# Kernel optimization log

Hardware: AMD Instinct MI355X
Metric: run time of the kernel (lower is better)

Reference implementation:

```python
import jax, jax.numpy as jnp
import numpy as np

HID = 2048
NKH, NVH = 16, 32
DK, DV = 128, 128
KCONV = 4
KEY_DIM = NKH * DK          # 2048
VAL_DIM = NVH * DV          # 4096
CONV_DIM = 2 * KEY_DIM + VAL_DIM  # 8192
QKVZ_DIM = 2 * KEY_DIM + 2 * VAL_DIM  # 12288
R = NVH // NKH              # 2
BA_DIM = 2 * NVH            # 64
EPS = 1e-6


def _l2norm(x, eps=1e-6):
    return x * jax.lax.rsqrt(jnp.sum(x * x, axis=-1, keepdims=True) + eps)


def setup_inputs() -> dict:
    key = jax.random.key(0)
    ks = jax.random.split(key, 8)
    std = 0.02
    return {
        "hidden_states": jax.random.normal(ks[0], (2, 2048, HID), dtype=jnp.float32),
        "attention_mask": jnp.ones((2, 2048), dtype=jnp.float32),
        "W_qkvz": jax.random.normal(ks[1], (HID, QKVZ_DIM), dtype=jnp.float32) * std,
        "W_ba": jax.random.normal(ks[2], (HID, BA_DIM), dtype=jnp.float32) * std,
        "conv_kernel": jax.random.normal(ks[3], (KCONV, 1, CONV_DIM), dtype=jnp.float32) * 0.1,
        "A_log": jnp.log(jax.random.uniform(ks[4], (NVH,), dtype=jnp.float32, minval=1.0, maxval=16.0)),
        "dt_bias": jnp.ones((NVH,), dtype=jnp.float32),
        "norm_kernel": jnp.ones((DV,), dtype=jnp.float32),
        "W_out": jax.random.normal(ks[5], (VAL_DIM, HID), dtype=jnp.float32) * std,
    }


def reference(hidden_states, attention_mask, W_qkvz, W_ba, conv_kernel, A_log, dt_bias, norm_kernel, W_out):
    b, s, _ = hidden_states.shape
    h = hidden_states * attention_mask[:, :, None]  # apply padding mask

    # projections
    qkvz = h @ W_qkvz  # (b, s, QKVZ_DIM)
    ba = h @ W_ba      # (b, s, BA_DIM)

    # fix_query_key_value_ordering: grouped per-k-head layout [q, k, v*R, z*R]
    qkvz = qkvz.reshape(b, s, NKH, 2 * DK + 2 * R * DV)
    q = qkvz[..., :DK]                                   # (b,s,NKH,DK)
    k = qkvz[..., DK:2 * DK]                             # (b,s,NKH,DK)
    v = qkvz[..., 2 * DK:2 * DK + R * DV].reshape(b, s, NVH, DV)
    z = qkvz[..., 2 * DK + R * DV:].reshape(b, s, NVH, DV)
    ba = ba.reshape(b, s, NKH, 2 * R)
    beta = ba[..., :R].reshape(b, s, NVH)
    alpha = ba[..., R:].reshape(b, s, NVH)

    # causal depthwise conv over [q|k|v] channels
    conv_in = jnp.concatenate(
        [q.reshape(b, s, -1), k.reshape(b, s, -1), v.reshape(b, s, -1)], axis=-1)  # (b,s,CONV_DIM)
    conv_out = jax.lax.conv_general_dilated(
        conv_in, conv_kernel, window_strides=(1,), padding=((KCONV - 1, 0),),
        dimension_numbers=("NWC", "WIO", "NWC"), feature_group_count=CONV_DIM)
    conv_out = jax.nn.silu(conv_out)

    q = conv_out[..., :KEY_DIM].reshape(b, s, NKH, DK)
    k = conv_out[..., KEY_DIM:2 * KEY_DIM].reshape(b, s, NKH, DK)
    v = conv_out[..., 2 * KEY_DIM:].reshape(b, s, NVH, DV)

    # expand k-heads to v-heads (repeat_interleave)
    q = jnp.repeat(q, R, axis=2)  # (b,s,NVH,DK)
    k = jnp.repeat(k, R, axis=2)

    # gated delta rule parameters
    g = -jnp.exp(A_log)[None, None, :] * jax.nn.softplus(alpha + dt_bias[None, None, :])  # (b,s,NVH)
    beta = jax.nn.sigmoid(beta)
    q = _l2norm(q) * (DK ** -0.5)
    k = _l2norm(k)

    # recurrence: S_t = exp(g_t) * S_{t-1} + k_t (v_t - k_t^T S) beta_t ; o_t = q_t^T S_t
    def step(S, x):
        q_t, k_t, v_t, g_t, b_t = x
        S = S * jnp.exp(g_t)[..., None, None]               # (b,h,DK,DV)
        kv = jnp.einsum("bhk,bhkv->bhv", k_t, S)
        delta = (v_t - kv) * b_t[..., None]
        S = S + jnp.einsum("bhk,bhv->bhkv", k_t, delta)
        o_t = jnp.einsum("bhk,bhkv->bhv", q_t, S)
        return S, o_t

    xs = (q.transpose(1, 0, 2, 3), k.transpose(1, 0, 2, 3), v.transpose(1, 0, 2, 3),
          g.transpose(1, 0, 2), beta.transpose(1, 0, 2))
    S0 = jnp.zeros((b, NVH, DK, DV), dtype=hidden_states.dtype)
    _, o = jax.lax.scan(step, S0, xs)
    o = o.transpose(1, 0, 2, 3)  # (b,s,NVH,DV)

    # gated RMSNorm per head (fp32 math as in Qwen3NextRMSNormGated)
    of = o.astype(jnp.float32)
    var = jnp.mean(of * of, axis=-1, keepdims=True)
    of = of * jax.lax.rsqrt(var + EPS)
    of = norm_kernel * of
    of = of * jax.nn.silu(z.astype(jnp.float32))
    o = of.astype(o.dtype).reshape(b, s, VAL_DIM)

    return o @ W_out
```

## Files before the change

kernel.cpp:

```cpp
#include <hip/hip_runtime.h>
#include <stdint.h>

typedef float    f32x4 __attribute__((ext_vector_type(4)));
typedef float    f32x2 __attribute__((ext_vector_type(2)));
typedef _Float16 f16x8 __attribute__((ext_vector_type(8)));
typedef _Float16 f16x4 __attribute__((ext_vector_type(4)));
typedef _Float16 f16x2 __attribute__((ext_vector_type(2)));

#define SEQ   2048
#define HIDD  2048
#define MROWS 4096
#define NQKV  12288
#define NCHUNK 32
#define CLEN   64

__device__ __forceinline__ void gload_lds16(const void* g, void* l) {
  __builtin_amdgcn_global_load_lds((const __attribute__((address_space(1))) uint32_t*)g,
                                   (__attribute__((address_space(3))) uint32_t*)l, 16, 0, 0);
}
__device__ __forceinline__ int swz256(int row, int colb) { return row * 256 + (colb ^ ((row & 7) << 4)); }
__device__ __forceinline__ int swz128(int row, int colb) { return row * 128 + (colb ^ ((row & 7) << 4)); }

__global__ __launch_bounds__(256)
void amask_kernel(const float* __restrict__ h, const float* __restrict__ mask,
                  _Float16* __restrict__ A1) {
  int i = blockIdx.x * 256 + threadIdx.x;
  if (i >= MROWS * HIDD / 4) return;
  f32x4 x = ((const f32x4*)h)[i];
  float m = mask[(i * 4) >> 11];
  f16x4 r;
  r[0] = (_Float16)(x[0] * m); r[1] = (_Float16)(x[1] * m);
  r[2] = (_Float16)(x[2] * m); r[3] = (_Float16)(x[3] * m);
  *(f16x4*)(A1 + (size_t)i * 4) = r;
}

__global__ __launch_bounds__(256)
void transpose_f16(const float* __restrict__ in, _Float16* __restrict__ out,
                   int R, int C) {
  __shared__ float tile[64][65];
  int c0 = blockIdx.x * 64, r0 = blockIdx.y * 64;
  int tx = threadIdx.x & 63, ty = threadIdx.x >> 6;
  #pragma unroll
  for (int i = 0; i < 16; ++i) {
    int r = i * 4 + ty;
    tile[r][tx] = in[(size_t)(r0 + r) * C + c0 + tx];
  }
  __syncthreads();
  #pragma unroll
  for (int i = 0; i < 16; ++i) {
    int c = i * 4 + ty;
    out[(size_t)(c0 + c) * R + r0 + tx] = (_Float16)tile[tx][c];
  }
}

template <typename CT>
__global__ __launch_bounds__(256, 2)
void gemm_f16(const _Float16* __restrict__ A, const _Float16* __restrict__ Bt,
              CT* __restrict__ C, int M, int N, int K, int tiles_n) {
  __shared__ _Float16 lsA[128 * 32];
  __shared__ _Float16 lsB[128 * 32];
  int bm = blockIdx.x / tiles_n, bn = blockIdx.x % tiles_n;
  int m0 = bm * 128, n0 = bn * 128;
  int lane = threadIdx.x & 63, wid = threadIdx.x >> 6;
  int wr = wid >> 1, wc = wid & 1;
  int la = lane & 15, lk = lane >> 4;
  int ldrow = lane >> 2;
  int ldcol = (lane & 3) * 8;
  f32x4 acc[4][4] = {};
  for (int k0 = 0; k0 < K; k0 += 32) {
    __syncthreads();
    #pragma unroll
    for (int si = 0; si < 2; ++si) {
      int seg = wid * 2 + si;
      int row = seg * 16 + ldrow;
      gload_lds16(A  + (size_t)(m0 + row) * K + k0 + ldcol, &lsA[seg * 512]);
      gload_lds16(Bt + (size_t)(n0 + row) * K + k0 + ldcol, &lsB[seg * 512]);
    }
    __syncthreads();
    f16x8 af[4], bf[4];
    #pragma unroll
    for (int f = 0; f < 4; ++f) {
      af[f] = *(const f16x8*)&lsA[(wr * 64 + f * 16 + la) * 32 + lk * 8];
      bf[f] = *(const f16x8*)&lsB[(wc * 64 + f * 16 + la) * 32 + lk * 8];
    }
    #pragma unroll
    for (int i = 0; i < 4; ++i)
      #pragma unroll
      for (int j = 0; j < 4; ++j)
        acc[i][j] = __builtin_amdgcn_mfma_f32_16x16x32_f16(af[i], bf[j], acc[i][j], 0, 0, 0);
  }
  #pragma unroll
  for (int i = 0; i < 4; ++i)
    #pragma unroll
    for (int j = 0; j < 4; ++j) {
      int col = n0 + wc * 64 + j * 16 + la;
      #pragma unroll
      for (int r = 0; r < 4; ++r) {
        int row = m0 + wr * 64 + i * 16 + lk * 4 + r;
        C[(size_t)row * N + col] = (CT)acc[i][j][r];
      }
    }
}

__global__ __launch_bounds__(256)
void ba_gemm(const float* __restrict__ h, const float* __restrict__ mask,
             const float* __restrict__ Wba, float* __restrict__ ba) {
  __shared__ float red[4][8][64];
  int r0 = blockIdx.x * 8;
  int c = threadIdx.x & 63, kc = threadIdx.x >> 6;
  float acc[8] = {};
  const float* wp = Wba + (size_t)(kc * 512) * 64 + c;
  const float* hp = h + (size_t)r0 * HIDD + kc * 512;
  for (int i = 0; i < 512; ++i) {
    float w = wp[(size_t)i * 64];
    #pragma unroll
    for (int r = 0; r < 8; ++r)
      acc[r] += hp[(size_t)r * HIDD + i] * w;
  }
  #pragma unroll
  for (int r = 0; r < 8; ++r) red[kc][r][c] = acc[r];
  __syncthreads();
  if (kc == 0) {
    #pragma unroll
    for (int r = 0; r < 8; ++r) {
      float s = red[0][r][c] + red[1][r][c] + red[2][r][c] + red[3][r][c];
      ba[(size_t)(r0 + r) * 64 + c] = s * mask[r0 + r];
    }
  }
}

__global__ __launch_bounds__(256)
void conv_kernel(const _Float16* __restrict__ qkvz, const float* __restrict__ ck,
                 _Float16* __restrict__ qn, _Float16* __restrict__ kn,
                 _Float16* __restrict__ vb) {
  int row = blockIdx.x;
  int b = row >> 11, t = row & 2047;
  int lane = threadIdx.x & 63, wid = threadIdx.x >> 6;
  for (int u = wid; u < 64; u += 4) {
    int c, cc, hh;
    if (u < 16)      { hh = u;      c = hh * 768;                               cc = hh * 128; }
    else if (u < 32) { hh = u - 16; c = hh * 768 + 128;                         cc = 2048 + hh * 128; }
    else             { hh = u - 32; c = (hh >> 1) * 768 + 256 + (hh & 1) * 128; cc = 4096 + hh * 128; }
    float y0 = 0.f, y1 = 0.f;
    #pragma unroll
    for (int j = 0; j < 4; ++j) {
      int tt = t - 3 + j;
      if (tt >= 0) {
        const _Float16* r = qkvz + (size_t)(b * 2048 + tt) * NQKV + c;
        f16x2 x = *(const f16x2*)(r + 2 * lane);
        f32x2 w = *(const f32x2*)(ck + j * 8192 + cc + 2 * lane);
        y0 += (float)x[0] * w[0];
        y1 += (float)x[1] * w[1];
      }
    }
    y0 = y0 / (1.f + expf(-y0));
    y1 = y1 / (1.f + expf(-y1));
    if (u < 32) {
      float ss = y0 * y0 + y1 * y1;
      #pragma unroll
      for (int m = 1; m < 64; m <<= 1) ss += __shfl_xor(ss, m);
      float rs = rsqrtf(ss + 1e-6f);
      if (u < 16) rs *= 0.08838834764831845f;
      y0 *= rs; y1 *= rs;
      _Float16* dst = (u < 16 ? qn : kn) + (size_t)row * 2048 + hh * 128;
      f16x2 o; o[0] = (_Float16)y0; o[1] = (_Float16)y1;
      *(f16x2*)(dst + 2 * lane) = o;
    } else {
      _Float16* dst = vb + (size_t)row * 4096 + hh * 128;
      f16x2 o; o[0] = (_Float16)y0; o[1] = (_Float16)y1;
      *(f16x2*)(dst + 2 * lane) = o;
    }
  }
}

__global__ __launch_bounds__(256)
void egbeta_kernel(const float* __restrict__ ba, const float* __restrict__ Alog,
                   const float* __restrict__ dtb, float* __restrict__ gout,
                   float* __restrict__ bout) {
  int i = blockIdx.x * 256 + threadIdx.x;
  if (i >= MROWS * 32) return;
  int vh = i >> 12, row = i & 4095;
  int kh = vh >> 1, r = vh & 1;
  const float* p = ba + (size_t)row * 64 + kh * 4;
  float bv = p[r], av = p[2 + r];
  float x = av + dtb[vh];
  float sp = (x > 20.f) ? x : log1pf(expf(x));
  gout[(size_t)vh * MROWS + row] = -expf(Alog[vh]) * sp;
  bout[(size_t)vh * MROWS + row] = 1.f / (1.f + expf(-bv));
}

__global__ __launch_bounds__(512, 2)
void chunk_scan(const _Float16* __restrict__ qn, const _Float16* __restrict__ kn,
                _Float16* __restrict__ vb, const float* __restrict__ gb,
                const float* __restrict__ btb) {
  __shared__ __align__(16) _Float16 Ks[64 * 128];
  __shared__ __align__(16) _Float16 Qs[64 * 128];
  __shared__ __align__(16) _Float16 Kt[128 * 64];
  __shared__ __align__(16) _Float16 Sf[32 * 128];
  __shared__ float AT[64 * 65];
  __shared__ __align__(16) _Float16 M16[64 * 64];
  __shared__ float RHS[32 * 65];
  __shared__ __align__(16) _Float16 Uv[32 * 64];
  __shared__ __align__(16) _Float16 Ub[32 * 64];
  __shared__ __align__(16) _Float16 Vb[64 * 32];
  __shared__ float gs[64], bs[64], cgs[64], bexp[64], scU[64];

  char* Ksb = (char*)Ks; char* Qsb = (char*)Qs; char* Ktb = (char*)Kt;
  char* Sfb = (char*)Sf; char* M16b = (char*)M16;
  char* Uvb = (char*)Uv; char* Ubb = (char*)Ub; char* Vbb = (char*)Vb;

  int bid = blockIdx.x;
  int b = bid >> 7, vh = (bid >> 2) & 31, vsl = bid & 3;
  int kh = vh >> 1;
  int tid = threadIdx.x;
  int w = tid >> 6, lane = tid & 63;
  int wr = w >> 1, wc = w & 1;
  int la = lane & 15, lk = lane >> 4;

  const _Float16* kgb = kn + (size_t)(b * 2048) * 2048 + kh * 128;
  const _Float16* qgb = qn + (size_t)(b * 2048) * 2048 + kh * 128;
  _Float16*       vgb = vb + (size_t)(b * 2048) * 4096 + vh * 128 + vsl * 32;
  const float*    ggb = gb  + (size_t)vh * MROWS + b * 2048;
  const float*    bgb = btb + (size_t)vh * MROWS + b * 2048;

  int srow = tid >> 3, sseg = tid & 7;
  int tk = tid & 127, tth = tid >> 7;

  f16x8 kr[2], qr[2]; f16x4 vr; float ebr;
  float sreg[2][4] = {};

  { f32x4 z = {}; ((f32x4*)Sf)[tid] = z; }

  kr[0] = *(const f16x8*)(kgb + (size_t)srow * 2048 + sseg * 16);
  kr[1] = *(const f16x8*)(kgb + (size_t)srow * 2048 + sseg * 16 + 8);
  qr[0] = *(const f16x8*)(qgb + (size_t)srow * 2048 + sseg * 16);
  qr[1] = *(const f16x8*)(qgb + (size_t)srow * 2048 + sseg * 16 + 8);
  vr    = *(const f16x4*)(vgb + (size_t)srow * 4096 + sseg * 4);
  ebr   = (tid < 64) ? ggb[tid] : (tid < 128 ? bgb[tid - 64] : 0.f);
  *(f16x8*)(Ksb + swz256(srow, sseg * 32))      = kr[0];
  *(f16x8*)(Ksb + swz256(srow, sseg * 32 + 16)) = kr[1];
  *(f16x8*)(Qsb + swz256(srow, sseg * 32))      = qr[0];
  *(f16x8*)(Qsb + swz256(srow, sseg * 32 + 16)) = qr[1];
  *(f16x4*)(Vbb + srow * 64 + sseg * 8) = vr;
  if (tid < 64) gs[tid] = ebr; else if (tid < 128) bs[tid - 64] = ebr;
  __syncthreads();

  #pragma unroll 1
  for (int c = 0; c < NCHUNK; ++c) {
    int cn = (c < NCHUNK - 1) ? c + 1 : c;
    kr[0] = *(const f16x8*)(kgb + (size_t)(cn * 64 + srow) * 2048 + sseg * 16);
    kr[1] = *(const f16x8*)(kgb + (size_t)(cn * 64 + srow) * 2048 + sseg * 16 + 8);
    qr[0] = *(const f16x8*)(qgb + (size_t)(cn * 64 + srow) * 2048 + sseg * 16);
    qr[1] = *(const f16x8*)(qgb + (size_t)(cn * 64 + srow) * 2048 + sseg * 16 + 8);
    vr    = *(const f16x4*)(vgb + (size_t)(cn * 64 + srow) * 4096 + sseg * 4);
    ebr   = (tid < 64) ? ggb[cn * 64 + tid] : (tid < 128 ? bgb[cn * 64 + tid - 64] : 0.f);

    f32x4 kk[2] = {}, qk[2] = {}, ks0 = {}, qs0 = {};
    #pragma unroll
    for (int ks = 0; ks < 4; ++ks) {
      f16x8 aK = *(const f16x8*)(Ksb + swz256(wr * 16 + la, ks * 64 + lk * 16));
      f16x8 aQ = *(const f16x8*)(Qsb + swz256(wr * 16 + la, ks * 64 + lk * 16));
      f16x8 bS = *(const f16x8*)(Sfb + swz256(wc * 16 + la, ks * 64 + lk * 16));
      #pragma unroll
      for (int j = 0; j < 2; ++j) {
        f16x8 bK = *(const f16x8*)(Ksb + swz256(wc * 32 + j * 16 + la, ks * 64 + lk * 16));
        kk[j] = __builtin_amdgcn_mfma_f32_16x16x32_f16(aK, bK, kk[j], 0, 0, 0);
        qk[j] = __builtin_amdgcn_mfma_f32_16x16x32_f16(aQ, bK, qk[j], 0, 0, 0);
      }
      ks0 = __builtin_amdgcn_mfma_f32_16x16x32_f16(aK, bS, ks0, 0, 0, 0);
      qs0 = __builtin_amdgcn_mfma_f32_16x16x32_f16(aQ, bS, qs0, 0, 0, 0);
    }
    {
      f16x8 r0, r1;
      #pragma unroll
      for (int j = 0; j < 8; ++j) {
        r0[j] = *(const _Float16*)(Ksb + swz256(tth * 16 + j, 2 * tk));
        r1[j] = *(const _Float16*)(Ksb + swz256(tth * 16 + 8 + j, 2 * tk));
      }
      *(f16x8*)(Ktb + swz128(tk, tth * 32))      = r0;
      *(f16x8*)(Ktb + swz128(tk, tth * 32 + 16)) = r1;
    }
    if (w == 0) {
      float g = gs[lane];
      #pragma unroll
      for (int off = 1; off < 64; off <<= 1) {
        float y = __shfl_up(g, off);
        if (lane >= off) g += y;
      }
      cgs[lane] = g;
      float cgL = __shfl(g, 63);
      bexp[lane] = __expf(g);
      scU[lane] = bs[lane] * __expf(cgL - g);
    }
    __syncthreads();

    {
      float cgt[4];
      #pragma unroll
      for (int r = 0; r < 4; ++r) cgt[r] = cgs[wr * 16 + lk * 4 + r];
      #pragma unroll
      for (int j = 0; j < 2; ++j) {
        int s = wc * 32 + j * 16 + la;
        float bsv = bs[s], cgss = cgs[s];
        #pragma unroll
        for (int r = 0; r < 4; ++r) {
          int t = wr * 16 + lk * 4 + r;
          float e = bsv * __expf(cgt[r] - cgss);
          AT[s * 65 + t] = (s < t) ? e * kk[j][r] : 0.f;
          float mm = (s <= t) ? e * qk[j][r] : 0.f;
          *(_Float16*)(M16b + swz128(t, s * 2)) = (_Float16)mm;
        }
      }
      #pragma unroll
      for (int r = 0; r < 4; ++r) {
        int t = wr * 16 + lk * 4 + r;
        int v = wc * 16 + la;
        float be = bexp[t];
        qs0[r] *= be;
        float vv = (float)*(const _Float16*)(Vbb + t * 64 + v * 2);
        RHS[v * 65 + t] = vv - be * ks0[r];
      }
    }
    __syncthreads();

    {
      float u[4];
      #pragma unroll
      for (int vi = 0; vi < 4; ++vi) u[vi] = RHS[(w * 4 + vi) * 65 + lane];
      #pragma unroll 1
      for (int sb = 0; sb < 8; ++sb) {
        float Ac[8];
        #pragma unroll
        for (int j = 0; j < 8; ++j) Ac[j] = AT[(sb * 8 + j) * 65 + lane];
        #pragma unroll
        for (int j = 0; j < 8; ++j) {
          int s = sb * 8 + j;
          #pragma unroll
          for (int vi = 0; vi < 4; ++vi) {
            float ubv = __builtin_bit_cast(float,
                __builtin_amdgcn_readlane(__builtin_bit_cast(int, u[vi]), s));
            u[vi] = fmaf(-Ac[j], ubv, u[vi]);
          }
        }
      }
      float sc = scU[lane];
      #pragma unroll
      for (int vi = 0; vi < 4; ++vi) {
        int v = w * 4 + vi;
        *(_Float16*)(Uvb + swz128(v, lane * 2)) = (_Float16)u[vi];
        *(_Float16*)(Ubb + swz128(v, lane * 2)) = (_Float16)(u[vi] * sc);
      }
    }
    __syncthreads();

    #pragma unroll
    for (int ss = 0; ss < 2; ++ss) {
      f16x8 aM = *(const f16x8*)(M16b + swz128(wr * 16 + la, ss * 64 + lk * 16));
      f16x8 bU = *(const f16x8*)(Uvb + swz128(wc * 16 + la, ss * 64 + lk * 16));
      qs0 = __builtin_amdgcn_mfma_f32_16x16x32_f16(aM, bU, qs0, 0, 0, 0);
    }
    #pragma unroll
    for (int r = 0; r < 4; ++r) {
      int t = wr * 16 + lk * 4 + r;
      vgb[(size_t)(c * 64 + t) * 4096 + wc * 16 + la] = (_Float16)qs0[r];
    }
    {
      f32x4 sd[2] = {};
      #pragma unroll
      for (int ss = 0; ss < 2; ++ss) {
        f16x8 bK = *(const f16x8*)(Ktb + swz128(w * 16 + la, ss * 64 + lk * 16));
        #pragma unroll
        for (int vt = 0; vt < 2; ++vt) {
          f16x8 aU = *(const f16x8*)(Ubb + swz128(vt * 16 + la, ss * 64 + lk * 16));
          sd[vt] = __builtin_amdgcn_mfma_f32_16x16x32_f16(aU, bK, sd[vt], 0, 0, 0);
        }
      }
      float beC = bexp[63];
      #pragma unroll
      for (int vt = 0; vt < 2; ++vt)
        #pragma unroll
        for (int r = 0; r < 4; ++r) {
          int v = vt * 16 + lk * 4 + r;
          int k = w * 16 + la;
          float sn = fmaf(sreg[vt][r], beC, sd[vt][r]);
          sreg[vt][r] = sn;
          *(_Float16*)(Sfb + swz256(v, k * 2)) = (_Float16)sn;
        }
    }
    __syncthreads();

    *(f16x8*)(Ksb + swz256(srow, sseg * 32))      = kr[0];
    *(f16x8*)(Ksb + swz256(srow, sseg * 32 + 16)) = kr[1];
    *(f16x8*)(Qsb + swz256(srow, sseg * 32))      = qr[0];
    *(f16x8*)(Qsb + swz256(srow, sseg * 32 + 16)) = qr[1];
    *(f16x4*)(Vbb + srow * 64 + sseg * 8) = vr;
    if (tid < 64) gs[tid] = ebr; else if (tid < 128) bs[tid - 64] = ebr;
    __syncthreads();
  }
}

__global__ __launch_bounds__(256)
void gate_kernel(const _Float16* __restrict__ ob, const _Float16* __restrict__ qkvz,
                 const float* __restrict__ nk, _Float16* __restrict__ Ag) {
  int row = blockIdx.x;
  int lane = threadIdx.x & 63, wid = threadIdx.x >> 6;
  for (int vh = wid; vh < 32; vh += 4) {
    const _Float16* op = ob + (size_t)row * 4096 + vh * 128;
    f16x2 xx = *(const f16x2*)(op + 2 * lane);
    float x0 = (float)xx[0], x1 = (float)xx[1];
    float ss = x0 * x0 + x1 * x1;
    #pragma unroll
    for (int m = 1; m < 64; m <<= 1) ss += __shfl_xor(ss, m);
    float rs = rsqrtf(ss * (1.f / 128.f) + 1e-6f);
    f32x2 nv = *(const f32x2*)(nk + 2 * lane);
    float v0 = x0 * rs * nv[0], v1 = x1 * rs * nv[1];
    const _Float16* zp = qkvz + (size_t)row * NQKV + (vh >> 1) * 768 + 512 + (vh & 1) * 128;
    f16x2 zz = *(const f16x2*)(zp + 2 * lane);
    float z0 = (float)zz[0], z1 = (float)zz[1];
    v0 *= z0 / (1.f + expf(-z0));
    v1 *= z1 / (1.f + expf(-z1));
    _Float16* dst = Ag + (size_t)row * 4096 + vh * 128;
    f16x2 o; o[0] = (_Float16)v0; o[1] = (_Float16)v1;
    *(f16x2*)(dst + 2 * lane) = o;
  }
}

extern "C" void kernel_launch(void* const* d_in, const int* in_sizes, int n_in,
                              void* d_out, int out_size, void* d_ws, size_t ws_size,
                              hipStream_t stream) {
  const float* h     = (const float*)d_in[0];
  const float* mask  = (const float*)d_in[1];
  const float* Wqkvz = (const float*)d_in[2];
  const float* Wba   = (const float*)d_in[3];
  const float* ck    = (const float*)d_in[4];
  const float* Alog  = (const float*)d_in[5];
  const float* dtb   = (const float*)d_in[6];
  const float* nk    = (const float*)d_in[7];
  const float* Wout  = (const float*)d_in[8];
  float* out = (float*)d_out;

  char* w = (char*)d_ws;
  const size_t o_qkvz = 0;
  const size_t o_A1   = 100663296;
  const size_t o_Bt1  = o_A1 + 16777216;
  const size_t o_ba   = o_Bt1 + 50331648;
  const size_t o_g    = o_ba + 1048576;
  const size_t o_bt   = o_g + 524288;
  const size_t total  = o_bt + 524288;
  if (ws_size < total) return;

  _Float16* qkvz16 = (_Float16*)(w + o_qkvz);
  _Float16* A1     = (_Float16*)(w + o_A1);
  _Float16* Bt1    = (_Float16*)(w + o_Bt1);
  float*    ba32   = (float*)   (w + o_ba);
  float*    gbuf   = (float*)   (w + o_g);
  float*    btb    = (float*)   (w + o_bt);
  _Float16* qn16 = (_Float16*)(w + o_A1);
  _Float16* kn16 = (_Float16*)(w + o_Bt1);
  _Float16* vb16 = (_Float16*)(w + o_Bt1 + 16777216);
  _Float16* Ag   = (_Float16*)(w + o_A1);
  _Float16* Wt2  = (_Float16*)(w + 0);

  amask_kernel<<<MROWS * HIDD / 4 / 256, 256, 0, stream>>>(h, mask, A1);
  transpose_f16<<<dim3(192, 32), 256, 0, stream>>>(Wqkvz, Bt1, HIDD, NQKV);
  ba_gemm<<<MROWS / 8, 256, 0, stream>>>(h, mask, Wba, ba32);
  gemm_f16<_Float16><<<32 * 96, 256, 0, stream>>>(A1, Bt1, qkvz16, MROWS, NQKV, HIDD, 96);
  conv_kernel<<<MROWS, 256, 0, stream>>>(qkvz16, ck, qn16, kn16, vb16);
  egbeta_kernel<<<MROWS * 32 / 256, 256, 0, stream>>>(ba32, Alog, dtb, gbuf, btb);
  chunk_scan<<<256, 512, 0, stream>>>(qn16, kn16, vb16, gbuf, btb);
  gate_kernel<<<MROWS, 256, 0, stream>>>(vb16, qkvz16, nk, Ag);
  transpose_f16<<<dim3(32, 64), 256, 0, stream>>>(Wout, Wt2, 4096, HIDD);
  gemm_f16<float><<<32 * 16, 256, 0, stream>>>(Ag, Wt2, out, MROWS, HIDD, 4096, 16);
}
```

Baseline: 782.9 us.

## Replace GEMM with 256x256 double-buffered swizzled-LDS tile kernel

Replaces the 128x128, K=32 single-buffered f16 MFMA GEMM with a 256x256-tile kernel using 512 threads, K=64 steps, double-buffered LDS prefetch via global_load_lds, and an XOR swizzle to avoid bank conflicts. Each wave now computes a 128x64 sub-tile, raising arithmetic intensity and overlapping global loads with MFMA work. Both projection GEMMs use it. The trade-offs are 128KB of LDS per block, which may limit occupancy to one block per CU, and far fewer blocks for the output GEMM (128 tiles), which may underfill the 256 CUs.

```diff
diff --git a/kernel.cpp b/kernel.cpp
--- a/kernel.cpp
+++ b/kernel.cpp
@@ -54,50 +54,78 @@
 }
 
 template <typename CT>
-__global__ __launch_bounds__(256, 2)
-void gemm_f16(const _Float16* __restrict__ A, const _Float16* __restrict__ Bt,
-              CT* __restrict__ C, int M, int N, int K, int tiles_n) {
-  __shared__ _Float16 lsA[128 * 32];
-  __shared__ _Float16 lsB[128 * 32];
+__global__ __launch_bounds__(512, 2)
+void gemm256(const _Float16* __restrict__ A, const _Float16* __restrict__ Bt,
+             CT* __restrict__ C, int M, int N, int K, int tiles_n) {
+  __shared__ __align__(16) _Float16 lsA[2][256 * 64];
+  __shared__ __align__(16) _Float16 lsB[2][256 * 64];
   int bm = blockIdx.x / tiles_n, bn = blockIdx.x % tiles_n;
-  int m0 = bm * 128, n0 = bn * 128;
-  int lane = threadIdx.x & 63, wid = threadIdx.x >> 6;
-  int wr = wid >> 1, wc = wid & 1;
+  int m0 = bm * 256, n0 = bn * 256;
+  int tid = threadIdx.x;
+  int w = tid >> 6, lane = tid & 63;
+  int wm = w >> 2, wn = w & 3;
   int la = lane & 15, lk = lane >> 4;
-  int ldrow = lane >> 2;
-  int ldcol = (lane & 3) * 8;
-  f32x4 acc[4][4] = {};
-  for (int k0 = 0; k0 < K; k0 += 32) {
+  int sr = lane >> 3;
+  int scb = ((lane & 7) << 4) ^ ((sr & 7) << 4);
+  int nkt = K >> 6;
+  f32x4 acc[8][4] = {};
+
+  {
+    const char* ga = (const char*)(A  + (size_t)(m0 + w * 32) * K);
+    const char* gb = (const char*)(Bt + (size_t)(n0 + w * 32) * K);
+    #pragma unroll
+    for (int i = 0; i < 4; ++i) {
+      gload_lds16(ga + (size_t)(i * 8 + sr) * (K * 2) + scb, &lsA[0][(w * 32 + i * 8) * 64]);
+      gload_lds16(gb + (size_t)(i * 8 + sr) * (K * 2) + scb, &lsB[0][(w * 32 + i * 8) * 64]);
+    }
+  }
+  __syncthreads();
+
+  int cur = 0;
+  for (int kt = 0; kt < nkt; ++kt) {
+    if (kt + 1 < nkt) {
+      const char* ga = (const char*)(A  + (size_t)(m0 + w * 32) * K + (kt + 1) * 64);
+      const char* gb = (const char*)(Bt + (size_t)(n0 + w * 32) * K + (kt + 1) * 64);
+      #pragma unroll
+      for (int i = 0; i < 4; ++i) {
+        gload_lds16(ga + (size_t)(i * 8 + sr) * (K * 2) + scb, &lsA[cur ^ 1][(w * 32 + i * 8) * 64]);
+        gload_lds16(gb + (size_t)(i * 8 + sr) * (K * 2) + scb, &lsB[cur ^ 1][(w * 32 + i * 8) * 64]);
+      }
+    }
+    const char* cA = (const char*)&lsA[cur][0];
+    const char* cB = (const char*)&lsB[cur][0];
+    #pragma unroll
+    for (int kw = 0; kw < 2; ++kw) {
+      f16x8 af[8], bf[4];
+      #pragma unroll
+      for (int f = 0; f < 8; ++f) {
+        int row = wm * 128 + f * 16 + la;
+        af[f] = *(const f16x8*)(cA + row * 128 + ((kw * 64 + lk * 16) ^ ((row & 7) << 4)));
+      }
+      #pragma unroll
+      for (int j = 0; j < 4; ++j) {
+        int row = wn * 64 + j * 16 + la;
+        bf[j] = *(const f16x8*)(cB + row * 128 + ((kw * 64 + lk * 16) ^ ((row & 7) << 4)));
+      }
+      #pragma unroll
+      for (int f = 0; f < 8; ++f)
+        #pragma unroll
+        for (int j = 0; j < 4; ++j)
+          acc[f][j] = __builtin_amdgcn_mfma_f32_16x16x32_f16(af[f], bf[j], acc[f][j], 0, 0, 0);
+    }
     __syncthreads();
-    #pragma unroll
-    for (int si = 0; si < 2; ++si) {
-      int seg = wid * 2 + si;
-      int row = seg * 16 + ldrow;
-      gload_lds16(A  + (size_t)(m0 + row) * K + k0 + ldcol, &lsA[seg * 512]);
-      gload_lds16(Bt + (size_t)(n0 + row) * K + k0 + ldcol, &lsB[seg * 512]);
-    }
-    __syncthreads();
-    f16x8 af[4], bf[4];
-    #pragma unroll
-    for (int f = 0; f < 4; ++f) {
-      af[f] = *(const f16x8*)&lsA[(wr * 64 + f * 16 + la) * 32 + lk * 8];
-      bf[f] = *(const f16x8*)&lsB[(wc * 64 + f * 16 + la) * 32 + lk * 8];
-    }
-    #pragma unroll
-    for (int i = 0; i < 4; ++i)
-      #pragma unroll
-      for (int j = 0; j < 4; ++j)
-        acc[i][j] = __builtin_amdgcn_mfma_f32_16x16x32_f16(af[i], bf[j], acc[i][j], 0, 0, 0);
-  }
+    cur ^= 1;
+  }
+
   #pragma unroll
-  for (int i = 0; i < 4; ++i)
+  for (int f = 0; f < 8; ++f)
     #pragma unroll
     for (int j = 0; j < 4; ++j) {
-      int col = n0 + wc * 64 + j * 16 + la;
+      int col = n0 + wn * 64 + j * 16 + la;
       #pragma unroll
       for (int r = 0; r < 4; ++r) {
-        int row = m0 + wr * 64 + i * 16 + lk * 4 + r;
-        C[(size_t)row * N + col] = (CT)acc[i][j][r];
+        int row = m0 + wm * 128 + f * 16 + lk * 4 + r;
+        C[(size_t)row * N + col] = (CT)acc[f][j][r];
       }
     }
 }
@@ -464,11 +492,11 @@
   amask_kernel<<<MROWS * HIDD / 4 / 256, 256, 0, stream>>>(h, mask, A1);
   transpose_f16<<<dim3(192, 32), 256, 0, stream>>>(Wqkvz, Bt1, HIDD, NQKV);
   ba_gemm<<<MROWS / 8, 256, 0, stream>>>(h, mask, Wba, ba32);
-  gemm_f16<_Float16><<<32 * 96, 256, 0, stream>>>(A1, Bt1, qkvz16, MROWS, NQKV, HIDD, 96);
+  gemm256<_Float16><<<16 * 48, 512, 0, stream>>>(A1, Bt1, qkvz16, MROWS, NQKV, HIDD, 48);
   conv_kernel<<<MROWS, 256, 0, stream>>>(qkvz16, ck, qn16, kn16, vb16);
   egbeta_kernel<<<MROWS * 32 / 256, 256, 0, stream>>>(ba32, Alog, dtb, gbuf, btb);
   chunk_scan<<<256, 512, 0, stream>>>(qn16, kn16, vb16, gbuf, btb);
   gate_kernel<<<MROWS, 256, 0, stream>>>(vb16, qkvz16, nk, Ag);
   transpose_f16<<<dim3(32, 64), 256, 0, stream>>>(Wout, Wt2, 4096, HIDD);
-  gemm_f16<float><<<32 * 16, 256, 0, stream>>>(Ag, Wt2, out, MROWS, HIDD, 4096, 16);
-}
+  gemm256<float><<<16 * 8, 512, 0, stream>>>(Ag, Wt2, out, MROWS, HIDD, 4096, 8);
+}
```

Result: faster. 744.7 us (-4.9%).
